# Performance work log

Measured on AMD Instinct MI355X. Metric: run time of the kernel, lower is better.

## Reference

```python
import jax, jax.numpy as jnp
import numpy as np

T, B, IN, H, F, OUT = 2048, 32, 256, 512, 2048, 256


def setup_inputs() -> dict:
    key = jax.random.key(0)
    ks = jax.random.split(key, 9)
    s_in = 1.0 / np.sqrt(IN)
    s_h = 1.0 / np.sqrt(H)
    s_f = 1.0 / np.sqrt(F)
    return {
        "x": jax.random.normal(ks[0], (T, B, IN), dtype=jnp.float32),
        "Wg": jax.random.uniform(ks[1], (H, IN), jnp.float32, -s_in, s_in),
        "bg": jax.random.uniform(ks[2], (H,), jnp.float32, -s_in, s_in),
        "Wi": jax.random.uniform(ks[3], (H, IN), jnp.float32, -s_in, s_in),
        "bi": jax.random.uniform(ks[4], (H,), jnp.float32, -s_in, s_in),
        "W1": jax.random.uniform(ks[5], (F, H), jnp.float32, -s_h, s_h),
        "b1": jax.random.uniform(ks[6], (F,), jnp.float32, -s_h, s_h),
        "W2": jax.random.uniform(ks[7], (OUT, F), jnp.float32, -s_f, s_f),
        "b2": jax.random.uniform(ks[8], (OUT,), jnp.float32, -s_f, s_f),
    }


def _gilr_scan(a, b):
    # h_t = a_t * h_{t-1} + b_t with h_0 = 0  ->  parallel associative scan over time
    def combine(c1, c2):
        a1, b1 = c1
        a2, b2 = c2
        return (a1 * a2, b1 * a2 + b2)
    _, h = jax.lax.associative_scan(combine, (a, b), axis=0)
    return h


def reference(x, Wg, bg, Wi, bi, W1, b1, W2, b2):
    # x: (T, B, IN)
    g = jax.nn.sigmoid(jnp.einsum("tbi,hi->tbh", x, Wg) + bg)  # (T,B,H)
    i = jnp.tanh(jnp.einsum("tbi,hi->tbh", x, Wi) + bi)        # (T,B,H)
    h = _gilr_scan(g, (1.0 - g) * i)                             # (T,B,H)
    z = jax.nn.gelu(jnp.einsum("tbh,fh->tbf", h, W1) + b1, approximate=False)
    out = jnp.einsum("tbf,of->tbo", z, W2) + b2                  # (T,B,OUT)
    return out
```

## Files before the change

kernel.cpp:

```cpp
#include <hip/hip_runtime.h>
#include <hip/hip_fp16.h>
#include <math.h>


#define IN_DIM 256
#define H_DIM 512
#define F_DIM 2048
#define OUT_DIM 256

typedef _Float16 f16;
typedef _Float16 f16x8 __attribute__((ext_vector_type(8)));
typedef float f32x4 __attribute__((ext_vector_type(4)));

#define AS3(p) ((__attribute__((address_space(3))) void*)(p))
#define AS1(p) ((const __attribute__((address_space(1))) void*)(p))
#define MFMA16(d, x, y) d = __builtin_amdgcn_mfma_f32_16x16x32_f16(x, y, d, 0, 0, 0)


__global__ void cvt_kernel(const float* __restrict__ in, f16* __restrict__ out, int n8) {
  int i = blockIdx.x * blockDim.x + threadIdx.x;
  if (i >= n8) return;
  const float4* p = (const float4*)in + (size_t)i * 2;
  float4 a = p[0], b = p[1];
  f16x8 o = { (f16)a.x, (f16)a.y, (f16)a.z, (f16)a.w,
              (f16)b.x, (f16)b.y, (f16)b.z, (f16)b.w };
  *((f16x8*)out + i) = o;
}

__global__ void cvt_w(const float* __restrict__ Wg, const float* __restrict__ Wi,
                      const float* __restrict__ W1, const float* __restrict__ W2,
                      f16* __restrict__ wgi, f16* __restrict__ w1, f16* __restrict__ w2) {
  int i = blockIdx.x * 256 + threadIdx.x;
  const float* src; f16* dst; int l;
  if (i < 16384)       { l = i;          src = Wg + (size_t)l * 8; dst = wgi + (size_t)l * 8; }
  else if (i < 32768)  { l = i - 16384;  src = Wi + (size_t)l * 8; dst = wgi + 131072 + (size_t)l * 8; }
  else if (i < 163840) { l = i - 32768;  src = W1 + (size_t)l * 8; dst = w1 + (size_t)l * 8; }
  else                 { l = i - 163840; src = W2 + (size_t)l * 8; dst = w2 + (size_t)l * 8; }
  float4 a = ((const float4*)src)[0], b = ((const float4*)src)[1];
  f16x8 o = { (f16)a.x, (f16)a.y, (f16)a.z, (f16)a.w,
              (f16)b.x, (f16)b.y, (f16)b.z, (f16)b.w };
  *(f16x8*)dst = o;
}

__global__ void bias_cat_kernel(const float* __restrict__ bg, const float* __restrict__ bi,
                                float* __restrict__ bgi) {
  int t = threadIdx.x;
  bgi[t] = (t < 512) ? bg[t] : bi[t - 512];
}

__device__ __forceinline__ float sigmoid_fast(float v) {
  return __builtin_amdgcn_rcpf(1.0f + __expf(-v));
}
__device__ __forceinline__ float tanh_fast(float v) {
  return 1.0f - 2.0f * __builtin_amdgcn_rcpf(__expf(2.0f * v) + 1.0f);
}
__device__ __forceinline__ float gelu_fast(float v) {
  float u = v * v;
  float y = v * fmaf(0.0713548353f, u, 1.59576912161f);
  return v * __builtin_amdgcn_rcpf(1.0f + __expf(-y));
}


__global__ __launch_bounds__(256, 5) void gemm1_k(
    const f16* __restrict__ A, const f16* __restrict__ Bw,
    const float* __restrict__ bias, f16* __restrict__ Cout) {
  constexpr int LDA = 256, LDB = 256, LDC = 1024, NT = 8;
  __shared__ f16 lds[2][2][128][32];
  const int tid = threadIdx.x, wid = tid >> 6, lane = tid & 63;
  const int bid = blockIdx.x;
  const int m0 = ((bid & 7) * 64 + (bid >> 6)) * 128;
  const int n0 = ((bid >> 3) & 7) * 128;
  const int wr = (wid >> 1) * 64, wc = (wid & 1) * 64;

  const f16* srcA[2]; const f16* srcB[2];
#pragma unroll
  for (int q = 0; q < 2; ++q) {
    int s = (wid * 2 + q) * 64 + lane;
    int row = s >> 2, g = (s & 3) ^ ((row >> 1) & 3);
    srcA[q] = A + (size_t)(m0 + row) * LDA + g * 8;
    srcB[q] = Bw + (size_t)(n0 + row) * LDB + g * 8;
  }
  auto stage = [&](int buf, int kt) {
    f16* la = &lds[buf][0][0][0] + (wid * 2) * 512;
    f16* lb = &lds[buf][1][0][0] + (wid * 2) * 512;
#pragma unroll
    for (int q = 0; q < 2; ++q) {
      __builtin_amdgcn_global_load_lds(AS1(srcA[q] + kt * 32), AS3(la + q * 512), 16, 0, 0);
      __builtin_amdgcn_global_load_lds(AS1(srcB[q] + kt * 32), AS3(lb + q * 512), 16, 0, 0);
    }
  };
  const int r = lane & 15;
  const int cs = (((lane >> 4) ^ ((lane >> 1) & 3)) << 3);

  f32x4 acc[4][4] = {};
  stage(0, 0);
  for (int kt = 0; kt < NT; ++kt) {
    __syncthreads();
    if (kt + 1 < NT) stage((kt + 1) & 1, kt + 1);
    f16(*At)[32] = lds[kt & 1][0];
    f16(*Bt)[32] = lds[kt & 1][1];
    f16x8 af[4], bf[4];
#pragma unroll
    for (int i = 0; i < 4; ++i) af[i] = *(const f16x8*)&At[wr + i * 16 + r][cs];
#pragma unroll
    for (int i = 0; i < 4; ++i) bf[i] = *(const f16x8*)&Bt[wc + i * 16 + r][cs];
#pragma unroll
    for (int mi = 0; mi < 4; ++mi)
#pragma unroll
      for (int ni = 0; ni < 4; ++ni)
        MFMA16(acc[mi][ni], af[mi], bf[ni]);
  }

  __syncthreads();
  const bool sig = n0 < 512;
  f16* ep = &lds[0][0][0][0] + wid * 4096;
  const int rq = (lane >> 4) * 4;
#pragma unroll
  for (int ni = 0; ni < 4; ++ni) {
    float bv = bias[n0 + wc + ni * 16 + r];
    int cc = ni * 2 + (r >> 3);
#pragma unroll
    for (int mi = 0; mi < 4; ++mi) {
#pragma unroll
      for (int j = 0; j < 4; ++j) {
        int lrow = mi * 16 + rq + j;
        float v = acc[mi][ni][j] + bv;
        float av = sig ? sigmoid_fast(v) : tanh_fast(v);
        ep[lrow * 64 + ((cc ^ (lrow & 7)) << 3) + (r & 7)] = (f16)av;
      }
    }
  }
  asm volatile("s_waitcnt lgkmcnt(0)" ::: "memory");
  __builtin_amdgcn_sched_barrier(0);
#pragma unroll
  for (int t = 0; t < 8; ++t) {
    int idx = t * 64 + lane;
    int row = idx >> 3, c = idx & 7;
    f16x8 v = *(const f16x8*)(ep + row * 64 + ((c ^ (row & 7)) << 3));
    *(f16x8*)(Cout + (size_t)(m0 + wr + row) * LDC + n0 + wc + c * 8) = v;
  }
}


#define GEMM2_BODY                                                                       \
  constexpr int LDA = 1024, LDB = 512, LDC = 2048, NT = 16;                              \
  __shared__ f16 lds[24576];                                                             \
  const int tid = threadIdx.x, wid = tid >> 6, lane = tid & 63;                          \
  const int lr = lane & 15;                                                              \
  const int bid = blockIdx.x;                                                            \
  const int m0 = ((bid & 7) * 8 + (bid >> 7)) * 256;                                     \
  const int n0 = ((bid >> 3) & 15) * 128;                                                \
  const int wr = (wid >> 1) * 128, wc = (wid & 1) * 64;                                  \
  const f16* srcA[4];                                                                    \
  const f16* srcB[2];                                                                    \
  _Pragma("unroll")                                                                      \
  for (int q = 0; q < 4; ++q) {                                                          \
    int s = wid * 256 + q * 64 + lane;                                                   \
    int row = s >> 2, g = (s & 3) ^ ((row >> 1) & 3);                                    \
    srcA[q] = A + (size_t)(m0 + row) * LDA + g * 8;                                      \
  }                                                                                      \
  _Pragma("unroll")                                                                      \
  for (int q = 0; q < 2; ++q) {                                                          \
    int s = wid * 128 + q * 64 + lane;                                                   \
    int row = s >> 2, g = (s & 3) ^ ((row >> 1) & 3);                                    \
    srcB[q] = Bw + (size_t)(n0 + row) * LDB + g * 8;                                     \
  }                                                                                      \
  auto stage = [&](int buf, int kt) {                                                    \
    _Pragma("unroll")                                                                    \
    for (int q = 0; q < 4; ++q)                                                          \
      __builtin_amdgcn_global_load_lds(AS1(srcA[q] + kt * 32),                           \
          AS3(lds + buf * 8192 + wid * 2048 + q * 512), 16, 0, 0);                       \
    _Pragma("unroll")                                                                    \
    for (int q = 0; q < 2; ++q)                                                          \
      __builtin_amdgcn_global_load_lds(AS1(srcB[q] + kt * 32),                           \
          AS3(lds + 16384 + buf * 4096 + wid * 1024 + q * 512), 16, 0, 0);               \
  };                                                                                     \
  const int qsf = (((lane >> 4) ^ ((lr >> 1) & 3)) << 3);                                \
  f32x4 acc[8][4] = {};                                                                  \
  stage(0, 0);                                                                           \
  for (int kt = 0; kt < NT; ++kt) {                                                      \
    const int cur = kt & 1;                                                              \
    __syncthreads();                                                                     \
    if (kt + 1 < NT) stage(cur ^ 1, kt + 1);                                             \
    f16x8 af[8], bf[4];                                                                  \
    _Pragma("unroll")                                                                    \
    for (int mi = 0; mi < 8; ++mi)                                                       \
      af[mi] = *(const f16x8*)(lds + cur * 8192 + (wr + mi * 16 + lr) * 32 + qsf);       \
    _Pragma("unroll")                                                                    \
    for (int ni = 0; ni < 4; ++ni)                                                       \
      bf[ni] = *(const f16x8*)(lds + 16384 + cur * 4096 + (wc + ni * 16 + lr) * 32 + qsf); \
    _Pragma("unroll")                                                                    \
    for (int mi = 0; mi < 8; ++mi)                                                       \
      _Pragma("unroll")                                                                  \
      for (int ni = 0; ni < 4; ++ni)                                                     \
        MFMA16(acc[mi][ni], af[mi], bf[ni]);                                             \
  }                                                                                      \
  __syncthreads();                                                                       \
  f16* ep = lds + wid * 4096;                                                            \
  const int rq = (lane >> 4) * 4;                                                        \
  _Pragma("unroll")                                                                      \
  for (int h = 0; h < 2; ++h) {                                                          \
    _Pragma("unroll")                                                                    \
    for (int mi = 0; mi < 4; ++mi) {                                                     \
      _Pragma("unroll")                                                                  \
      for (int ni = 0; ni < 4; ++ni) {                                                   \
        float bv = bias[n0 + wc + ni * 16 + lr];                                         \
        int cc = ni * 2 + (lr >> 3);                                                     \
        _Pragma("unroll")                                                                \
        for (int j = 0; j < 4; ++j) {                                                    \
          int lrow = mi * 16 + rq + j;                                                   \
          float v = gelu_fast(acc[h * 4 + mi][ni][j] + bv);                              \
          ep[lrow * 64 + ((cc ^ (lrow & 7)) << 3) + (lr & 7)] = (f16)v;                  \
        }                                                                                \
      }                                                                                  \
    }                                                                                    \
    asm volatile("s_waitcnt lgkmcnt(0)" ::: "memory");                                   \
    __builtin_amdgcn_sched_barrier(0);                                                   \
    _Pragma("unroll")                                                                    \
    for (int t = 0; t < 8; ++t) {                                                        \
      int idx = t * 64 + lane;                                                           \
      int row = idx >> 3, c = idx & 7;                                                   \
      f16x8 v = *(const f16x8*)(ep + row * 64 + ((c ^ (row & 7)) << 3));                 \
      *(f16x8*)(Cout + (size_t)(m0 + wr + h * 64 + row) * LDC + n0 + wc + c * 8) = v;    \
    }                                                                                    \
    asm volatile("s_waitcnt lgkmcnt(0)" ::: "memory");                                   \
    __builtin_amdgcn_sched_barrier(0);                                                   \
  }

__global__ __launch_bounds__(256, 3) void gemm2_k3(
    const f16* __restrict__ A, const f16* __restrict__ Bw,
    const float* __restrict__ bias, f16* __restrict__ Cout) {
  GEMM2_BODY
}
__global__ __launch_bounds__(256, 2) void gemm2_k2(
    const f16* __restrict__ A, const f16* __restrict__ Bw,
    const float* __restrict__ bias, f16* __restrict__ Cout) {
  GEMM2_BODY
}
#undef GEMM2_BODY


__global__ __launch_bounds__(256, 2) void gemm3_k(
    const f16* __restrict__ A, const f16* __restrict__ Bw,
    const float* __restrict__ bias, float* __restrict__ Cout) {
  constexpr int LDA = 2048, LDB = 2048, LDC = 256, NT = 32;
  __shared__ f16 lds[2][2][128][64];
  const int tid = threadIdx.x, wid = tid >> 6, lane = tid & 63;
  const int bid = blockIdx.x;
  const int m0 = ((bid & 7) * 16 + (bid >> 4)) * 128;
  const int n0 = ((bid >> 3) & 1) * 128;
  const int wr = (wid >> 1) * 64, wc = (wid & 1) * 64;

  auto stage = [&](int buf, int kt) {
    const f16* ga = A + (size_t)m0 * LDA + kt * 64;
    const f16* gb = Bw + (size_t)n0 * LDB + kt * 64;
    f16* la = &lds[buf][0][0][0];
    f16* lb = &lds[buf][1][0][0];
#pragma unroll
    for (int q = 0; q < 4; ++q) {
      int seg = (wid << 2) + q;
      int s = seg * 64 + lane;
      int row = s >> 3, col = (s & 7) << 3;
      __builtin_amdgcn_global_load_lds(AS1(ga + (size_t)row * LDA + col),
                                       AS3(la + seg * 512), 16, 0, 0);
      __builtin_amdgcn_global_load_lds(AS1(gb + (size_t)row * LDB + col),
                                       AS3(lb + seg * 512), 16, 0, 0);
    }
  };

  f32x4 acc[4][4] = {};
  stage(0, 0);
  for (int kt = 0; kt < NT; ++kt) {
    __syncthreads();
    if (kt + 1 < NT) stage((kt + 1) & 1, kt + 1);
    f16(*At)[64] = lds[kt & 1][0];
    f16(*Bt)[64] = lds[kt & 1][1];
    const int r = lane & 15, cg = (lane >> 4) << 3;
#pragma unroll
    for (int kk = 0; kk < 2; ++kk) {
      f16x8 af[4], bf[4];
#pragma unroll
      for (int i = 0; i < 4; ++i)
        af[i] = *(const f16x8*)&At[wr + i * 16 + r][kk * 32 + cg];
#pragma unroll
      for (int i = 0; i < 4; ++i)
        bf[i] = *(const f16x8*)&Bt[wc + i * 16 + r][kk * 32 + cg];
#pragma unroll
      for (int mi = 0; mi < 4; ++mi)
#pragma unroll
        for (int ni = 0; ni < 4; ++ni)
          MFMA16(acc[mi][ni], af[mi], bf[ni]);
    }
  }
  const int r = lane & 15, rq = (lane >> 4) * 4;
#pragma unroll
  for (int ni = 0; ni < 4; ++ni) {
    int col = n0 + wc + ni * 16 + r;
    float bv = bias[col];
#pragma unroll
    for (int mi = 0; mi < 4; ++mi) {
#pragma unroll
      for (int j = 0; j < 4; ++j) {
        int row = m0 + wr + mi * 16 + rq + j;
        Cout[(size_t)row * LDC + col] = acc[mi][ni][j] + bv;
      }
    }
  }
}


#define NCH 16384
#define NCHUNK 32
#define CLEN 64

__global__ void scan_p1(const f16* __restrict__ ab, float* __restrict__ cA,
                        float* __restrict__ cH) {
  int ch = blockIdx.x * 256 + threadIdx.x;
  int c = blockIdx.y;
  const f16* pg = ab + (size_t)(c * CLEN) * 32768 + (ch >> 9) * 1024 + (ch & 511);
  const f16* pi = pg + 512;
  float A = 1.f, Hl = 0.f;
  for (int t = 0; t < CLEN; ++t) {
    float g = (float)pg[0];
    float ii = (float)pi[0];
    Hl = fmaf(g, Hl - ii, ii);
    A *= g;
    pg += 32768; pi += 32768;
  }
  cA[c * NCH + ch] = A;
  cH[c * NCH + ch] = Hl;
}

__global__ void scan_p2(const float* __restrict__ cA, const float* __restrict__ cH,
                        float* __restrict__ st) {
  int ch = blockIdx.x * 256 + threadIdx.x;
  float h0 = 0.f;
  for (int c = 0; c < NCHUNK; ++c) {
    st[c * NCH + ch] = h0;
    h0 = cA[c * NCH + ch] * h0 + cH[c * NCH + ch];
  }
}

__global__ void scan_p3(f16* __restrict__ ab, const float* __restrict__ st) {
  int ch = blockIdx.x * 256 + threadIdx.x;
  int c = blockIdx.y;
  f16* pg = ab + (size_t)(c * CLEN) * 32768 + (ch >> 9) * 1024 + (ch & 511);
  const f16* pi = pg + 512;
  float hv = st[c * NCH + ch];
  for (int t = 0; t < CLEN; ++t) {
    float g = (float)pg[0];
    float ii = (float)pi[0];
    hv = fmaf(g, hv - ii, ii);
    pg[0] = (f16)hv;
    pg += 32768; pi += 32768;
  }
}


extern "C" void kernel_launch(void* const* d_in, const int* in_sizes, int n_in,
                              void* d_out, int out_size, void* d_ws, size_t ws_size,
                              hipStream_t stream) {
  const float* x  = (const float*)d_in[0];
  const float* Wg = (const float*)d_in[1];
  const float* bg = (const float*)d_in[2];
  const float* Wi = (const float*)d_in[3];
  const float* bi = (const float*)d_in[4];
  const float* W1 = (const float*)d_in[5];
  const float* b1 = (const float*)d_in[6];
  const float* W2 = (const float*)d_in[7];
  const float* b2 = (const float*)d_in[8];
  float* out = (float*)d_out;

  char* ws = (char*)d_ws;
  f16*   wgi16 = (f16*)(ws + 0);
  f16*   w116  = (f16*)(ws + 524288);
  f16*   w216  = (f16*)(ws + 2621440);
  float* bgi   = (float*)(ws + 3670016);
  f16*   x16   = (f16*)(ws + 4194304);
  f16*   ab16  = (f16*)(ws + 37748736);
  float* cA    = (float*)(ws + 171966464);
  float* cH    = (float*)(ws + 174063616);
  float* st    = (float*)(ws + 176160768);
  f16*   z16   = (f16*)(ws + 178257920);
  if (ws_size < 245366784) return;

  cvt_w<<<896, 256, 0, stream>>>(Wg, Wi, W1, W2, wgi16, w116, w216);
  bias_cat_kernel<<<1, 1024, 0, stream>>>(bg, bi, bgi);
  cvt_kernel<<<8192, 256, 0, stream>>>(x, x16, 2097152);

  gemm1_k<<<4096, 256, 0, stream>>>(x16, wgi16, bgi, ab16);

  scan_p1<<<dim3(64, NCHUNK), 256, 0, stream>>>(ab16, cA, cH);
  scan_p2<<<64, 256, 0, stream>>>(cA, cH, st);
  scan_p3<<<dim3(64, NCHUNK), 256, 0, stream>>>(ab16, st);

  for (int s = 0; s < 4; ++s) {
    const f16* hs = ab16 + (size_t)s * 16384 * 1024;
    if (s < 2)
      gemm2_k3<<<1024, 256, 0, stream>>>(hs, w116, b1, z16);
    else
      gemm2_k2<<<1024, 256, 0, stream>>>(hs, w116, b1, z16);
    gemm3_k<<<256, 256, 0, stream>>>(z16, w216, b2, out + (size_t)s * 16384 * 256);
  }
}
```

Before: 520.0 us.

## Split gemm1 into two variants, add setprio to gemm2, narrow gemm3 tiles

gemm1 now runs as two launches over the two halves of M: one is the original double-buffered kernel with occupancy hint 4, the other a triple-buffered variant with explicit vmcnt waits. One gemm2 variant raises wave priority around its MFMA block, and both gemm2 variants now use a launch bound of 3. gemm3 halves its N tile to 64, doubling the grid to 512 blocks to improve CU fill. The split halves are odd experiments that mainly seem aimed at comparing variants, and the extra launches add overhead.

```diff
diff --git a/kernel.cpp b/kernel.cpp
--- a/kernel.cpp
+++ b/kernel.cpp
@@ -61,14 +61,14 @@
 }
 
 
-__global__ __launch_bounds__(256, 5) void gemm1_k(
+__global__ __launch_bounds__(256, 4) void gemm1_t2(
     const f16* __restrict__ A, const f16* __restrict__ Bw,
     const float* __restrict__ bias, f16* __restrict__ Cout) {
   constexpr int LDA = 256, LDB = 256, LDC = 1024, NT = 8;
   __shared__ f16 lds[2][2][128][32];
   const int tid = threadIdx.x, wid = tid >> 6, lane = tid & 63;
   const int bid = blockIdx.x;
-  const int m0 = ((bid & 7) * 64 + (bid >> 6)) * 128;
+  const int m0 = ((bid & 7) * 32 + (bid >> 6)) * 128;
   const int n0 = ((bid >> 3) & 7) * 128;
   const int wr = (wid >> 1) * 64, wc = (wid & 1) * 64;
 
@@ -142,7 +142,95 @@
 }
 
 
-#define GEMM2_BODY                                                                       \
+__global__ __launch_bounds__(256, 3) void gemm1_t3(
+    const f16* __restrict__ A, const f16* __restrict__ Bw,
+    const float* __restrict__ bias, f16* __restrict__ Cout) {
+  constexpr int LDA = 256, LDB = 256, LDC = 1024, NT = 8;
+  __shared__ f16 lds[3][2][128][32];
+  const int tid = threadIdx.x, wid = tid >> 6, lane = tid & 63;
+  const int bid = blockIdx.x;
+  const int m0 = ((bid & 7) * 32 + (bid >> 6)) * 128;
+  const int n0 = ((bid >> 3) & 7) * 128;
+  const int wr = (wid >> 1) * 64, wc = (wid & 1) * 64;
+
+  const f16* srcA[2]; const f16* srcB[2];
+#pragma unroll
+  for (int q = 0; q < 2; ++q) {
+    int s = (wid * 2 + q) * 64 + lane;
+    int row = s >> 2, g = (s & 3) ^ ((row >> 1) & 3);
+    srcA[q] = A + (size_t)(m0 + row) * LDA + g * 8;
+    srcB[q] = Bw + (size_t)(n0 + row) * LDB + g * 8;
+  }
+  auto stage = [&](int buf, int kt) {
+    f16* la = &lds[buf][0][0][0] + (wid * 2) * 512;
+    f16* lb = &lds[buf][1][0][0] + (wid * 2) * 512;
+#pragma unroll
+    for (int q = 0; q < 2; ++q) {
+      __builtin_amdgcn_global_load_lds(AS1(srcA[q] + kt * 32), AS3(la + q * 512), 16, 0, 0);
+      __builtin_amdgcn_global_load_lds(AS1(srcB[q] + kt * 32), AS3(lb + q * 512), 16, 0, 0);
+    }
+  };
+  const int r = lane & 15;
+  const int cs = (((lane >> 4) ^ ((lane >> 1) & 3)) << 3);
+
+  f32x4 acc[4][4] = {};
+  stage(0, 0); stage(1, 1);
+  asm volatile("s_waitcnt vmcnt(4)" ::: "memory");
+  __syncthreads();
+#pragma unroll
+  for (int kt = 0; kt < NT; ++kt) {
+    if (kt + 2 < NT) stage((kt + 2) % 3, kt + 2);
+    f16(*At)[32] = lds[kt % 3][0];
+    f16(*Bt)[32] = lds[kt % 3][1];
+    f16x8 af[4], bf[4];
+#pragma unroll
+    for (int i = 0; i < 4; ++i) af[i] = *(const f16x8*)&At[wr + i * 16 + r][cs];
+#pragma unroll
+    for (int i = 0; i < 4; ++i) bf[i] = *(const f16x8*)&Bt[wc + i * 16 + r][cs];
+#pragma unroll
+    for (int mi = 0; mi < 4; ++mi)
+#pragma unroll
+      for (int ni = 0; ni < 4; ++ni)
+        MFMA16(acc[mi][ni], af[mi], bf[ni]);
+    if (kt + 1 < NT) {
+      if (kt + 2 < NT) asm volatile("s_waitcnt vmcnt(4)" ::: "memory");
+      else             asm volatile("s_waitcnt vmcnt(0)" ::: "memory");
+      __syncthreads();
+    }
+  }
+
+  __syncthreads();
+  const bool sig = n0 < 512;
+  f16* ep = &lds[0][0][0][0] + wid * 4096;
+  const int rq = (lane >> 4) * 4;
+#pragma unroll
+  for (int ni = 0; ni < 4; ++ni) {
+    float bv = bias[n0 + wc + ni * 16 + r];
+    int cc = ni * 2 + (r >> 3);
+#pragma unroll
+    for (int mi = 0; mi < 4; ++mi) {
+#pragma unroll
+      for (int j = 0; j < 4; ++j) {
+        int lrow = mi * 16 + rq + j;
+        float v = acc[mi][ni][j] + bv;
+        float av = sig ? sigmoid_fast(v) : tanh_fast(v);
+        ep[lrow * 64 + ((cc ^ (lrow & 7)) << 3) + (r & 7)] = (f16)av;
+      }
+    }
+  }
+  asm volatile("s_waitcnt lgkmcnt(0)" ::: "memory");
+  __builtin_amdgcn_sched_barrier(0);
+#pragma unroll
+  for (int t = 0; t < 8; ++t) {
+    int idx = t * 64 + lane;
+    int row = idx >> 3, c = idx & 7;
+    f16x8 v = *(const f16x8*)(ep + row * 64 + ((c ^ (row & 7)) << 3));
+    *(f16x8*)(Cout + (size_t)(m0 + wr + row) * LDC + n0 + wc + c * 8) = v;
+  }
+}
+
+
+#define GEMM2_BODY(SETPRIO)                                                              \
   constexpr int LDA = 1024, LDB = 512, LDC = 2048, NT = 16;                              \
   __shared__ f16 lds[24576];                                                             \
   const int tid = threadIdx.x, wid = tid >> 6, lane = tid & 63;                          \
@@ -189,11 +277,13 @@
     _Pragma("unroll")                                                                    \
     for (int ni = 0; ni < 4; ++ni)                                                       \
       bf[ni] = *(const f16x8*)(lds + 16384 + cur * 4096 + (wc + ni * 16 + lr) * 32 + qsf); \
+    if (SETPRIO) __builtin_amdgcn_s_setprio(1);                                          \
     _Pragma("unroll")                                                                    \
     for (int mi = 0; mi < 8; ++mi)                                                       \
       _Pragma("unroll")                                                                  \
       for (int ni = 0; ni < 4; ++ni)                                                     \
         MFMA16(acc[mi][ni], af[mi], bf[ni]);                                             \
+    if (SETPRIO) __builtin_amdgcn_s_setprio(0);                                          \
   }                                                                                      \
   __syncthreads();                                                                       \
   f16* ep = lds + wid * 4096;                                                            \
@@ -227,74 +317,78 @@
     __builtin_amdgcn_sched_barrier(0);                                                   \
   }
 
-__global__ __launch_bounds__(256, 3) void gemm2_k3(
+__global__ __launch_bounds__(256, 3) void gemm2_a(
     const f16* __restrict__ A, const f16* __restrict__ Bw,
     const float* __restrict__ bias, f16* __restrict__ Cout) {
-  GEMM2_BODY
-}
-__global__ __launch_bounds__(256, 2) void gemm2_k2(
+  GEMM2_BODY(0)
+}
+__global__ __launch_bounds__(256, 3) void gemm2_s(
     const f16* __restrict__ A, const f16* __restrict__ Bw,
     const float* __restrict__ bias, f16* __restrict__ Cout) {
-  GEMM2_BODY
+  GEMM2_BODY(1)
 }
 #undef GEMM2_BODY
 
 
-__global__ __launch_bounds__(256, 2) void gemm3_k(
+__global__ __launch_bounds__(256, 2) void gemm3_h(
     const f16* __restrict__ A, const f16* __restrict__ Bw,
     const float* __restrict__ bias, float* __restrict__ Cout) {
   constexpr int LDA = 2048, LDB = 2048, LDC = 256, NT = 32;
-  __shared__ f16 lds[2][2][128][64];
+  __shared__ f16 lds[24576];
   const int tid = threadIdx.x, wid = tid >> 6, lane = tid & 63;
   const int bid = blockIdx.x;
-  const int m0 = ((bid & 7) * 16 + (bid >> 4)) * 128;
-  const int n0 = ((bid >> 3) & 1) * 128;
-  const int wr = (wid >> 1) * 64, wc = (wid & 1) * 64;
+  const int m0 = ((bid & 7) * 16 + (bid >> 5)) * 128;
+  const int n0 = ((bid >> 3) & 3) * 64;
+  const int wr = (wid >> 1) * 64, wc = (wid & 1) * 32;
 
   auto stage = [&](int buf, int kt) {
     const f16* ga = A + (size_t)m0 * LDA + kt * 64;
     const f16* gb = Bw + (size_t)n0 * LDB + kt * 64;
-    f16* la = &lds[buf][0][0][0];
-    f16* lb = &lds[buf][1][0][0];
 #pragma unroll
     for (int q = 0; q < 4; ++q) {
-      int seg = (wid << 2) + q;
+      int seg = wid * 4 + q;
       int s = seg * 64 + lane;
       int row = s >> 3, col = (s & 7) << 3;
       __builtin_amdgcn_global_load_lds(AS1(ga + (size_t)row * LDA + col),
-                                       AS3(la + seg * 512), 16, 0, 0);
+                                       AS3(lds + buf * 8192 + seg * 512), 16, 0, 0);
+    }
+#pragma unroll
+    for (int q = 0; q < 2; ++q) {
+      int seg = wid * 2 + q;
+      int s = seg * 64 + lane;
+      int row = s >> 3, col = (s & 7) << 3;
       __builtin_amdgcn_global_load_lds(AS1(gb + (size_t)row * LDB + col),
-                                       AS3(lb + seg * 512), 16, 0, 0);
+                                       AS3(lds + 16384 + buf * 4096 + seg * 512), 16, 0, 0);
     }
   };
 
-  f32x4 acc[4][4] = {};
+  f32x4 acc[4][2] = {};
   stage(0, 0);
   for (int kt = 0; kt < NT; ++kt) {
     __syncthreads();
     if (kt + 1 < NT) stage((kt + 1) & 1, kt + 1);
-    f16(*At)[64] = lds[kt & 1][0];
-    f16(*Bt)[64] = lds[kt & 1][1];
+    const f16* At = lds + (kt & 1) * 8192;
+    const f16* Bt = lds + 16384 + (kt & 1) * 4096;
     const int r = lane & 15, cg = (lane >> 4) << 3;
 #pragma unroll
     for (int kk = 0; kk < 2; ++kk) {
-      f16x8 af[4], bf[4];
+      f16x8 af[4], bf[2];
 #pragma unroll
       for (int i = 0; i < 4; ++i)
-        af[i] = *(const f16x8*)&At[wr + i * 16 + r][kk * 32 + cg];
-#pragma unroll
-      for (int i = 0; i < 4; ++i)
-        bf[i] = *(const f16x8*)&Bt[wc + i * 16 + r][kk * 32 + cg];
+        af[i] = *(const f16x8*)(At + (wr + i * 16 + r) * 64 + kk * 32 + cg);
+#pragma unroll
+      for (int i = 0; i < 2; ++i)
+        bf[i] = *(const f16x8*)(Bt + (wc + i * 16 + r) * 64 + kk * 32 + cg);
 #pragma unroll
       for (int mi = 0; mi < 4; ++mi)
 #pragma unroll
-        for (int ni = 0; ni < 4; ++ni)
+        for (int ni = 0; ni < 2; ++ni)
           MFMA16(acc[mi][ni], af[mi], bf[ni]);
     }
   }
   const int r = lane & 15, rq = (lane >> 4) * 4;
 #pragma unroll
-  for (int ni = 0; ni < 4; ++ni) {
+  for (int ni = 0; ni < 2; ++ni) {
     int col = n0 + wc + ni * 16 + r;
     float bv = bias[col];
 #pragma unroll
@@ -388,7 +482,9 @@
   bias_cat_kernel<<<1, 1024, 0, stream>>>(bg, bi, bgi);
   cvt_kernel<<<8192, 256, 0, stream>>>(x, x16, 2097152);
 
-  gemm1_k<<<4096, 256, 0, stream>>>(x16, wgi16, bgi, ab16);
+  gemm1_t2<<<2048, 256, 0, stream>>>(x16, wgi16, bgi, ab16);
+  gemm1_t3<<<2048, 256, 0, stream>>>(x16 + (size_t)32768 * 256, wgi16, bgi,
+                                     ab16 + (size_t)32768 * 1024);
 
   scan_p1<<<dim3(64, NCHUNK), 256, 0, stream>>>(ab16, cA, cH);
   scan_p2<<<64, 256, 0, stream>>>(cA, cH, st);
@@ -397,9 +493,9 @@
   for (int s = 0; s < 4; ++s) {
     const f16* hs = ab16 + (size_t)s * 16384 * 1024;
     if (s < 2)
-      gemm2_k3<<<1024, 256, 0, stream>>>(hs, w116, b1, z16);
+      gemm2_a<<<1024, 256, 0, stream>>>(hs, w116, b1, z16);
     else
-      gemm2_k2<<<1024, 256, 0, stream>>>(hs, w116, b1, z16);
-    gemm3_k<<<256, 256, 0, stream>>>(z16, w216, b2, out + (size_t)s * 16384 * 256);
-  }
-}
+      gemm2_s<<<1024, 256, 0, stream>>>(hs, w116, b1, z16);
+    gemm3_h<<<512, 256, 0, stream>>>(z16, w216, b2, out + (size_t)s * 16384 * 256);
+  }
+}
```

New measurement: 686.7 us. 32.0% more time.
